# Kernel optimization log

Hardware: AMD Instinct MI355X
Metric: run time of the kernel (lower is better)

The kernel has to match this reference:

```python
import jax, jax.numpy as jnp
import numpy as np

MAX_POINTS = 32
EPS = 1e-5


def setup_inputs() -> dict:
    key = jax.random.key(0)
    k1, k2, k3, k4, k5, k6 = jax.random.split(key, 6)
    M, P, C_IN, C_OUT = 40000, MAX_POINTS, 4, 64
    voxel_features = jax.random.normal(k1, (M, P, C_IN), dtype=jnp.float32)
    voxel_num_points = jax.random.randint(k2, (M,), 0, MAX_POINTS, dtype=jnp.int32)
    # Linear(C_in, C_out) params (PyTorch default init scale ~ U(-1/sqrt(fan_in), ...))
    lim = 1.0 / np.sqrt(C_IN)
    W = jax.random.uniform(k3, (C_OUT, C_IN), minval=-lim, maxval=lim, dtype=jnp.float32)
    b = jax.random.uniform(k4, (C_OUT,), minval=-lim, maxval=lim, dtype=jnp.float32)
    # BatchNorm1d affine params
    gamma = jnp.ones((C_OUT,), dtype=jnp.float32)
    beta = jnp.zeros((C_OUT,), dtype=jnp.float32)
    return {"voxel_features": voxel_features, "voxel_num_points": voxel_num_points,
            "W": W, "b": b, "gamma": gamma, "beta": beta}


def _vfe(x, n, W, b, gamma, beta):
    # x: (M, P, C_in), n: (M,) valid point counts
    mask = (jnp.arange(MAX_POINTS)[None, :] < n[:, None])            # (M, P)
    maskf = mask.astype(x.dtype)[..., None]                          # (M, P, 1)
    h = jnp.einsum('mpc,oc->mpo', x, W) + b                          # (M, P, C_out)
    h = h * maskf                                                    # zero invalid slots
    # BatchNorm1d (training-mode batch stats) over valid points only
    n_valid = jnp.maximum(jnp.sum(maskf), 1.0)
    mu = jnp.sum(h, axis=(0, 1)) / n_valid                           # (C_out,)
    d = (h - mu) * maskf
    var = jnp.sum(d * d, axis=(0, 1)) / n_valid                      # biased var, as BN
    hn = d * jax.lax.rsqrt(var + EPS) * gamma + beta * maskf
    hn = jax.nn.relu(hn) * maskf
    # per-voxel mean over valid points; voxels with n==0 output zeros
    counts = jnp.maximum(n.astype(x.dtype), 1.0)[:, None]
    return jnp.sum(hn, axis=1) / counts                              # (M, C_out)


def reference(voxel_features, voxel_num_points, W, b, gamma, beta):
    return _vfe(voxel_features, voxel_num_points, W, b, gamma, beta)
```

## Files before the change

kernel.cpp:

```cpp
#include <hip/hip_runtime.h>

#define MAX_POINTS 32
#define C_OUT 64
#define EPS 1e-5f

#define NMOM 15
#define NSET 8

__global__ __launch_bounds__(256) void vfe_stats(
    const float* __restrict__ x, const int* __restrict__ vnp,
    float* __restrict__ ws, int M)
{
    const int tid    = blockIdx.x * 256 + threadIdx.x;
    const int stride = gridDim.x * 256;
    const int total  = M * MAX_POINTS;

    float a[NMOM];
    #pragma unroll
    for (int i = 0; i < NMOM; ++i) a[i] = 0.f;

    const float4* __restrict__ xq = (const float4*)x;
    for (int i = tid; i < total; i += stride) {
        const float4 q0 = xq[i];
        const int   n   = vnp[i >> 5];
        const float mk  = ((i & 31) < n) ? 1.f : 0.f;
        const float qx = q0.x * mk, qy = q0.y * mk, qz = q0.z * mk, qw = q0.w * mk;
        a[0] += qx; a[1] += qy; a[2] += qz; a[3] += qw;
        a[4]  = fmaf(qx, qx, a[4]);
        a[5]  = fmaf(qx, qy, a[5]);
        a[6]  = fmaf(qx, qz, a[6]);
        a[7]  = fmaf(qx, qw, a[7]);
        a[8]  = fmaf(qy, qy, a[8]);
        a[9]  = fmaf(qy, qz, a[9]);
        a[10] = fmaf(qy, qw, a[10]);
        a[11] = fmaf(qz, qz, a[11]);
        a[12] = fmaf(qz, qw, a[12]);
        a[13] = fmaf(qw, qw, a[13]);
        a[14] += mk;
    }

    #pragma unroll
    for (int i = 0; i < NMOM; ++i) {
        float v = a[i];
        #pragma unroll
        for (int off = 32; off > 0; off >>= 1)
            v += __shfl_down(v, off, 64);
        a[i] = v;
    }

    __shared__ float bl[4][NMOM];
    const int lane = threadIdx.x & 63;
    const int wid  = threadIdx.x >> 6;
    if (lane == 0) {
        #pragma unroll
        for (int i = 0; i < NMOM; ++i) bl[wid][i] = a[i];
    }
    __syncthreads();
    if (threadIdx.x < NMOM) {
        const int i = threadIdx.x;
        const int set = blockIdx.x & (NSET - 1);
        atomicAdd(&ws[set * 16 + i], bl[0][i] + bl[1][i] + bl[2][i] + bl[3][i]);
    }
}

template<int NP>
__device__ __forceinline__ float voxel_body(
    const float4* __restrict__ xq, int n,
    float4 w4, float bias, float A, float B)
{
    float acc0 = 0.f, acc1 = 0.f, acc2 = 0.f, acc3 = 0.f;
    #pragma unroll
    for (int p = 0; p < NP; ++p) {
        const float4 q = xq[p];
        const float h = fmaf(q.x, w4.x, fmaf(q.y, w4.y,
                        fmaf(q.z, w4.z, fmaf(q.w, w4.w, bias))));
        float v = fmaxf(fmaf(h, A, B), 0.f);
        if (p >= NP - 8) v = (p < n) ? v : 0.f;
        if      ((p & 3) == 0) acc0 += v;
        else if ((p & 3) == 1) acc1 += v;
        else if ((p & 3) == 2) acc2 += v;
        else                   acc3 += v;
    }
    return (acc0 + acc1) + (acc2 + acc3);
}

__global__ __launch_bounds__(256) void vfe_out(
    const float* __restrict__ x, const int* __restrict__ vnp,
    const float* __restrict__ W, const float* __restrict__ b,
    const float* __restrict__ gamma, const float* __restrict__ beta,
    const float* __restrict__ ws, float* __restrict__ out, int M)
{
    const int lane = threadIdx.x & 63;
    const int wid  = threadIdx.x >> 6;
    const int gw   = blockIdx.x * 4 + wid;

    const float4* __restrict__ ws4 = (const float4*)ws;
    float4 m4[4];
    #pragma unroll
    for (int k = 0; k < 4; ++k) {
        float4 s = ws4[k];
        #pragma unroll
        for (int j = 1; j < NSET; ++j) {
            const float4 t = ws4[j * 4 + k];
            s.x += t.x; s.y += t.y; s.z += t.z; s.w += t.w;
        }
        m4[k] = s;
    }
    const float mom[NMOM] = { m4[0].x, m4[0].y, m4[0].z, m4[0].w,
                              m4[1].x, m4[1].y, m4[1].z, m4[1].w,
                              m4[2].x, m4[2].y, m4[2].z, m4[2].w,
                              m4[3].x, m4[3].y, m4[3].z };

    const float4 w4  = ((const float4*)W)[lane];
    const float bias = b[lane];
    const float cnt  = mom[14];
    const float nv   = fmaxf(cnt, 1.0f);
    const float wdots = w4.x*mom[0] + w4.y*mom[1] + w4.z*mom[2] + w4.w*mom[3];
    const float mu   = (wdots + cnt * bias) / nv;
    const float q2 = mom[4]*w4.x*w4.x + mom[8]*w4.y*w4.y + mom[11]*w4.z*w4.z + mom[13]*w4.w*w4.w
                   + 2.f*(mom[5]*w4.x*w4.y + mom[6]*w4.x*w4.z + mom[7]*w4.x*w4.w
                        + mom[9]*w4.y*w4.z + mom[10]*w4.y*w4.w + mom[12]*w4.z*w4.w);
    const float SS  = q2 + 2.f*bias*wdots + cnt*bias*bias;
    const float var = fmaxf(SS / nv - mu * mu, 0.f);
    const float A   = gamma[lane] * rsqrtf(var + EPS);
    const float B   = fmaf(-mu, A, beta[lane]);

    const int m_base = gw * 4;
    #pragma unroll
    for (int v = 0; v < 4; ++v) {
        const int m = m_base + v;
        if (m >= M) break;
        const int n = vnp[m];
        const float4* __restrict__ xq = (const float4*)x + (size_t)m * MAX_POINTS;
        float acc;
        if      (n > 24) acc = voxel_body<32>(xq, n, w4, bias, A, B);
        else if (n > 16) acc = voxel_body<24>(xq, n, w4, bias, A, B);
        else if (n >  8) acc = voxel_body<16>(xq, n, w4, bias, A, B);
        else if (n >  0) acc = voxel_body< 8>(xq, n, w4, bias, A, B);
        else             acc = 0.f;
        const float rn = 1.0f / fmaxf((float)n, 1.0f);
        out[(size_t)m * C_OUT + lane] = acc * rn;
    }
}

extern "C" void kernel_launch(void* const* d_in, const int* in_sizes, int n_in,
                              void* d_out, int out_size, void* d_ws, size_t ws_size,
                              hipStream_t stream) {
    const float* x     = (const float*)d_in[0];
    const int*   vnp   = (const int*)  d_in[1];
    const float* W     = (const float*)d_in[2];
    const float* b     = (const float*)d_in[3];
    const float* gamma = (const float*)d_in[4];
    const float* beta  = (const float*)d_in[5];
    float* out = (float*)d_out;
    float* ws  = (float*)d_ws;
    const int M = in_sizes[1];

    hipMemsetAsync(d_ws, 0, NSET * 16 * sizeof(float), stream);
    vfe_stats<<<2048, 256, 0, stream>>>(x, vnp, ws, M);
    const int nwaves = (M + 3) / 4;
    const int nblk   = (nwaves + 3) / 4;
    vfe_out<<<nblk, 256, 0, stream>>>(x, vnp, W, b, gamma, beta, ws, out, M);
}
```

Before: 117.7 us.

## Finalize BN moments in last stats block and fold affine into weights

The stats kernel now spreads atomics over more slots, runs on fewer blocks, and uses a last-block-done counter so one block reduces the partial moment sets into a single final vector. The output kernel then reads only 16 floats instead of summing every set in each wave. The per-point linear, BN scale and shift are folded into pre-scaled weights plus one constant, which saves one FMA per point. Voxel counts are loaded once as an int4. The cost is an extra threadfence, an extra atomic and a serial final reduction at the end of the stats kernel.

```diff
diff --git a/kernel.cpp b/kernel.cpp
--- a/kernel.cpp
+++ b/kernel.cpp
@@ -5,7 +5,12 @@
 #define EPS 1e-5f
 
 #define NMOM 15
-#define NSET 8
+#define NSET 32
+#define CNT_IDX (NSET * 16)
+#define FIN_IDX (NSET * 16 + 16)
+#define WS_FLOATS (NSET * 16 + 32)
+
+#define STATS_BLOCKS 1024
 
 __global__ __launch_bounds__(256) void vfe_stats(
     const float* __restrict__ x, const int* __restrict__ vnp,
@@ -49,6 +54,7 @@
     }
 
     __shared__ float bl[4][NMOM];
+    __shared__ int   is_last;
     const int lane = threadIdx.x & 63;
     const int wid  = threadIdx.x >> 6;
     if (lane == 0) {
@@ -56,25 +62,51 @@
         for (int i = 0; i < NMOM; ++i) bl[wid][i] = a[i];
     }
     __syncthreads();
+    const int set = blockIdx.x & (NSET - 1);
     if (threadIdx.x < NMOM) {
         const int i = threadIdx.x;
-        const int set = blockIdx.x & (NSET - 1);
         atomicAdd(&ws[set * 16 + i], bl[0][i] + bl[1][i] + bl[2][i] + bl[3][i]);
+    }
+    __threadfence();
+    __syncthreads();
+    if (threadIdx.x == 0) {
+        const int old = atomicAdd((int*)&ws[CNT_IDX], 1);
+        is_last = (old == gridDim.x - 1);
+    }
+    __syncthreads();
+
+    if (is_last && threadIdx.x < 64) {
+        const int s = threadIdx.x;
+        float v[NMOM];
+        #pragma unroll
+        for (int i = 0; i < NMOM; ++i)
+            v[i] = (s < NSET) ? atomicAdd(&ws[s * 16 + i], 0.0f) : 0.f;
+        #pragma unroll
+        for (int i = 0; i < NMOM; ++i) {
+            float t = v[i];
+            #pragma unroll
+            for (int off = 32; off > 0; off >>= 1)
+                t += __shfl_down(t, off, 64);
+            v[i] = t;
+        }
+        if (threadIdx.x == 0) {
+            #pragma unroll
+            for (int i = 0; i < NMOM; ++i) ws[FIN_IDX + i] = v[i];
+        }
     }
 }
 
 template<int NP>
 __device__ __forceinline__ float voxel_body(
-    const float4* __restrict__ xq, int n,
-    float4 w4, float bias, float A, float B)
+    const float4* __restrict__ xq, int n, float4 wA, float c0)
 {
     float acc0 = 0.f, acc1 = 0.f, acc2 = 0.f, acc3 = 0.f;
     #pragma unroll
     for (int p = 0; p < NP; ++p) {
         const float4 q = xq[p];
-        const float h = fmaf(q.x, w4.x, fmaf(q.y, w4.y,
-                        fmaf(q.z, w4.z, fmaf(q.w, w4.w, bias))));
-        float v = fmaxf(fmaf(h, A, B), 0.f);
+        float v = fmaf(q.x, wA.x, fmaf(q.y, wA.y,
+                  fmaf(q.z, wA.z, fmaf(q.w, wA.w, c0))));
+        v = fmaxf(v, 0.f);
         if (p >= NP - 8) v = (p < n) ? v : 0.f;
         if      ((p & 3) == 0) acc0 += v;
         else if ((p & 3) == 1) acc1 += v;
@@ -94,22 +126,12 @@
     const int wid  = threadIdx.x >> 6;
     const int gw   = blockIdx.x * 4 + wid;
 
-    const float4* __restrict__ ws4 = (const float4*)ws;
-    float4 m4[4];
-    #pragma unroll
-    for (int k = 0; k < 4; ++k) {
-        float4 s = ws4[k];
-        #pragma unroll
-        for (int j = 1; j < NSET; ++j) {
-            const float4 t = ws4[j * 4 + k];
-            s.x += t.x; s.y += t.y; s.z += t.z; s.w += t.w;
-        }
-        m4[k] = s;
-    }
-    const float mom[NMOM] = { m4[0].x, m4[0].y, m4[0].z, m4[0].w,
-                              m4[1].x, m4[1].y, m4[1].z, m4[1].w,
-                              m4[2].x, m4[2].y, m4[2].z, m4[2].w,
-                              m4[3].x, m4[3].y, m4[3].z };
+    const float4* __restrict__ wsf = (const float4*)(ws + FIN_IDX);
+    const float4 f0 = wsf[0], f1 = wsf[1], f2 = wsf[2], f3 = wsf[3];
+    const float mom[NMOM] = { f0.x, f0.y, f0.z, f0.w,
+                              f1.x, f1.y, f1.z, f1.w,
+                              f2.x, f2.y, f2.z, f2.w,
+                              f3.x, f3.y, f3.z };
 
     const float4 w4  = ((const float4*)W)[lane];
     const float bias = b[lane];
@@ -124,19 +146,34 @@
     const float var = fmaxf(SS / nv - mu * mu, 0.f);
     const float A   = gamma[lane] * rsqrtf(var + EPS);
     const float B   = fmaf(-mu, A, beta[lane]);
+    const float4 wA = make_float4(w4.x * A, w4.y * A, w4.z * A, w4.w * A);
+    const float  c0 = fmaf(bias, A, B);
 
     const int m_base = gw * 4;
+    if (m_base >= M) return;
+
+    int4 n4;
+    if (m_base + 3 < M) {
+        n4 = *(const int4*)(vnp + m_base);
+    } else {
+        n4.x = vnp[m_base];
+        n4.y = (m_base + 1 < M) ? vnp[m_base + 1] : 0;
+        n4.z = (m_base + 2 < M) ? vnp[m_base + 2] : 0;
+        n4.w = (m_base + 3 < M) ? vnp[m_base + 3] : 0;
+    }
+    const int ns[4] = { n4.x, n4.y, n4.z, n4.w };
+
     #pragma unroll
     for (int v = 0; v < 4; ++v) {
         const int m = m_base + v;
         if (m >= M) break;
-        const int n = vnp[m];
+        const int n = ns[v];
         const float4* __restrict__ xq = (const float4*)x + (size_t)m * MAX_POINTS;
         float acc;
-        if      (n > 24) acc = voxel_body<32>(xq, n, w4, bias, A, B);
-        else if (n > 16) acc = voxel_body<24>(xq, n, w4, bias, A, B);
-        else if (n >  8) acc = voxel_body<16>(xq, n, w4, bias, A, B);
-        else if (n >  0) acc = voxel_body< 8>(xq, n, w4, bias, A, B);
+        if      (n > 24) acc = voxel_body<32>(xq, n, wA, c0);
+        else if (n > 16) acc = voxel_body<24>(xq, n, wA, c0);
+        else if (n >  8) acc = voxel_body<16>(xq, n, wA, c0);
+        else if (n >  0) acc = voxel_body< 8>(xq, n, wA, c0);
         else             acc = 0.f;
         const float rn = 1.0f / fmaxf((float)n, 1.0f);
         out[(size_t)m * C_OUT + lane] = acc * rn;
@@ -156,8 +193,8 @@
     float* ws  = (float*)d_ws;
     const int M = in_sizes[1];
 
-    hipMemsetAsync(d_ws, 0, NSET * 16 * sizeof(float), stream);
-    vfe_stats<<<2048, 256, 0, stream>>>(x, vnp, ws, M);
+    hipMemsetAsync(d_ws, 0, WS_FLOATS * sizeof(float), stream);
+    vfe_stats<<<STATS_BLOCKS, 256, 0, stream>>>(x, vnp, ws, M);
     const int nwaves = (M + 3) / 4;
     const int nblk   = (nwaves + 3) / 4;
     vfe_out<<<nblk, 256, 0, stream>>>(x, vnp, W, b, gamma, beta, ws, out, M);
```

Measured after the change: 165.8 us. 40.9% more time.
